# Optimization experiments

Hardware: AMD Instinct MI355X
Metric: run time of the kernel (lower is better)

Reference implementation:

```python
import jax, jax.numpy as jnp
import numpy as np

N_NODES = 100000
N_EDGES = 1600000
NODE_DIM = 64
HIDDEN = 256
OUT_DIM = 64
BN_EPS = 1e-5


def setup_inputs() -> dict:
    key = jax.random.key(0)
    ks = jax.random.split(key, 6)
    h = jax.random.normal(ks[0], (N_NODES, NODE_DIM), dtype=jnp.float32)
    W1 = jax.random.normal(ks[1], (NODE_DIM, HIDDEN), dtype=jnp.float32) * 0.1
    b1 = jnp.zeros((HIDDEN,), dtype=jnp.float32)
    W2 = jax.random.normal(ks[2], (HIDDEN, OUT_DIM), dtype=jnp.float32) * 0.1
    b2 = jnp.zeros((OUT_DIM,), dtype=jnp.float32)
    gamma = jnp.ones((OUT_DIM,), dtype=jnp.float32)
    beta = jnp.zeros((OUT_DIM,), dtype=jnp.float32)
    src = jax.random.randint(ks[3], (N_EDGES,), 0, N_NODES, dtype=jnp.int32)
    dst = jax.random.randint(ks[4], (N_EDGES,), 0, N_NODES, dtype=jnp.int32)
    return {"h": h, "W1": W1, "b1": b1, "W2": W2, "b2": b2,
            "gamma": gamma, "beta": beta, "src": src, "dst": dst}


def reference(h, W1, b1, W2, b2, gamma, beta, src, dst):
    # --- mean aggregation over incoming neighbors (DGL update_all) ---
    # mailbox mean == segment_sum(h[src]) / in_degree(dst), zero for isolated nodes
    agg_sum = jax.ops.segment_sum(h[src], dst, num_segments=N_NODES)  # [N, d]
    deg = jax.ops.segment_sum(jnp.ones((src.shape[0],), h.dtype), dst,
                              num_segments=N_NODES)
    agg = agg_sum / jnp.clip(deg, 1.0, None)[:, None]
    x = agg + h  # GIN combine: aggregated msg + self feature
    # --- 2-layer MLP with relu, then final relu (node_update_fn) ---
    x = jax.nn.relu(x @ W1 + b1)
    x = x @ W2 + b2
    x = jax.nn.relu(x)
    # --- BatchNorm1d over node (batch) dimension, training-mode stats ---
    mean = jnp.mean(x, axis=0)
    var = jnp.var(x, axis=0)  # biased variance, as torch BN training
    x = (x - mean) * jax.lax.rsqrt(var + BN_EPS) * gamma + beta
    return x
```

## Files before the change

kernel.cpp:

```cpp
#include <hip/hip_runtime.h>

#define N_NODES 100000
#define N_EDGES 1600000
#define DIM     64
#define HID     256
#define BN_EPS  1e-5f

#define NBUCK   391
#define RSTRIDE 392
#define SCHUNK  3125
#define SBLK    512
#define MAXB    6144

#define XBROWS  100032
#define NGP     782
#define MLPGRID 256
#define MAXIT   4

typedef short bf16x8 __attribute__((ext_vector_type(8)));
typedef float f32x4  __attribute__((ext_vector_type(4)));


__device__ __forceinline__ unsigned short f2bf(float x) {
    unsigned int u = __float_as_uint(x);
    unsigned int r = (u + 0x7FFFu + ((u >> 16) & 1u)) >> 16;
    return (unsigned short)r;
}

#define WAITV(N) asm volatile("s_waitcnt vmcnt(" #N ")" ::: "memory")

__device__ __forceinline__ void stage_issue(const unsigned short* gsrc,
                                            unsigned short* ldst) {
    __builtin_amdgcn_global_load_lds(
        (const __attribute__((address_space(1))) void*)gsrc,
        (__attribute__((address_space(3))) void*)ldst, 16, 0, 0);
    __builtin_amdgcn_global_load_lds(
        (const __attribute__((address_space(1))) void*)(gsrc + 512),
        (__attribute__((address_space(3))) void*)(ldst + 512), 16, 0, 0);
}

__global__ __launch_bounds__(1024) void kA_scatter(const int* __restrict__ src,
                                                   const int* __restrict__ dst,
                                                   unsigned int* __restrict__ ebuf,
                                                   int* __restrict__ runoff) {
    __shared__ int hist[NBUCK];
    __shared__ int ebase[NBUCK];
    __shared__ int sc[512];
    __shared__ unsigned int stage[SCHUNK];
    const int t = threadIdx.x;
    const int e0 = blockIdx.x * SCHUNK;
    const int n = SCHUNK;

    for (int i = t; i < NBUCK; i += 1024) hist[i] = 0;
    __syncthreads();
    for (int i = t; i < n; i += 1024)
        atomicAdd(&hist[dst[e0 + i] >> 8], 1);
    __syncthreads();

    if (t < 512) sc[t] = (t < NBUCK) ? hist[t] : 0;
    __syncthreads();
    for (int off = 1; off < 512; off <<= 1) {
        int add = (t < 512 && t >= off) ? sc[t - off] : 0;
        __syncthreads();
        if (t < 512) sc[t] += add;
        __syncthreads();
    }
    if (t < NBUCK) {
        int ex = sc[t] - hist[t];
        ebase[t] = ex;
        runoff[blockIdx.x * RSTRIDE + t] = ex;
    }
    if (t == 0) runoff[blockIdx.x * RSTRIDE + NBUCK] = n;
    if (t < NBUCK) hist[t] = 0;
    __syncthreads();

    for (int i = t; i < n; i += 1024) {
        int d = dst[e0 + i];
        int s = src[e0 + i];
        int b = d >> 8;
        int r = atomicAdd(&hist[b], 1);
        stage[ebase[b] + r] = ((unsigned int)s << 8) | (unsigned int)(d & 255);
    }
    __syncthreads();
    for (int i = t; i < n; i += 1024)
        ebuf[e0 + i] = stage[i];
}

__global__ __launch_bounds__(1024) void kB_fused(const unsigned int* __restrict__ ebuf,
                                                 const int* __restrict__ runoff,
                                                 const unsigned short* __restrict__ hb,
                                                 unsigned short* __restrict__ xb) {
    __shared__ int runbase[SBLK + 1];
    __shared__ int runstart[SBLK];
    __shared__ int sc[SBLK];
    __shared__ int cnt[256];
    __shared__ int off[256];
    __shared__ unsigned int stage2[MAXB];
    __shared__ unsigned int sout[MAXB];
    const int t = threadIdx.x;
    const int b = blockIdx.x;

    int rl = 0;
    if (t < SBLK) {
        int s = runoff[t * RSTRIDE + b];
        int e = runoff[t * RSTRIDE + b + 1];
        runstart[t] = t * SCHUNK + s;
        rl = e - s;
        sc[t] = rl;
    }
    if (t < 256) cnt[t] = 0;
    __syncthreads();
    for (int o = 1; o < SBLK; o <<= 1) {
        int add = (t < SBLK && t >= o) ? sc[t - o] : 0;
        __syncthreads();
        if (t < SBLK) sc[t] += add;
        __syncthreads();
    }
    if (t < SBLK) runbase[t] = sc[t] - rl;
    if (t == 0) runbase[SBLK] = sc[SBLK - 1];
    __syncthreads();
    const int total = min(runbase[SBLK], MAXB);

    for (int idx = t; idx < total; idx += 1024) {
        int lo = 0, hi = SBLK - 1;
        while (lo < hi) {
            int mid = (lo + hi + 1) >> 1;
            if (runbase[mid] <= idx) lo = mid; else hi = mid - 1;
        }
        unsigned int v = ebuf[runstart[lo] + (idx - runbase[lo])];
        stage2[idx] = v;
        atomicAdd(&cnt[v & 255u], 1);
    }
    __syncthreads();

    int c0 = (t < 256) ? cnt[t] : 0;
    if (t < 256) sc[t] = c0;
    __syncthreads();
    for (int o = 1; o < 256; o <<= 1) {
        int add = (t < 256 && t >= o) ? sc[t - o] : 0;
        __syncthreads();
        if (t < 256) sc[t] += add;
        __syncthreads();
    }
    if (t < 256) { off[t] = sc[t] - c0; cnt[t] = 0; }
    __syncthreads();

    for (int idx = t; idx < total; idx += 1024) {
        unsigned int v = stage2[idx];
        int node = (int)(v & 255u);
        int r = atomicAdd(&cnt[node], 1);
        sout[off[node] + r] = v >> 8;
    }
    __syncthreads();

    const int g = t >> 3, c = t & 7;
    const unsigned short* hc = hb + c * 8;
    const int gn0 = b * 256;
#pragma unroll
    for (int pass = 0; pass < 2; ++pass) {
        int nloc = pass * 128 + g;
        int gnode = gn0 + nloc;
        if (gnode >= N_NODES) continue;
        const int o0 = off[nloc];
        const int dg = cnt[nloc];
        float a0 = 0.f, a1 = 0.f, a2 = 0.f, a3 = 0.f;
        float a4 = 0.f, a5 = 0.f, a6 = 0.f, a7 = 0.f;
        int j = 0;
        for (; j + 1 < dg; j += 2) {
            int i0 = (int)sout[o0 + j];
            int i1 = (int)sout[o0 + j + 1];
            uint4 v0 = *(const uint4*)&hc[(size_t)i0 * 64];
            uint4 v1 = *(const uint4*)&hc[(size_t)i1 * 64];
            a0 += __uint_as_float(v0.x << 16); a1 += __uint_as_float(v0.x & 0xffff0000u);
            a2 += __uint_as_float(v0.y << 16); a3 += __uint_as_float(v0.y & 0xffff0000u);
            a4 += __uint_as_float(v0.z << 16); a5 += __uint_as_float(v0.z & 0xffff0000u);
            a6 += __uint_as_float(v0.w << 16); a7 += __uint_as_float(v0.w & 0xffff0000u);
            a0 += __uint_as_float(v1.x << 16); a1 += __uint_as_float(v1.x & 0xffff0000u);
            a2 += __uint_as_float(v1.y << 16); a3 += __uint_as_float(v1.y & 0xffff0000u);
            a4 += __uint_as_float(v1.z << 16); a5 += __uint_as_float(v1.z & 0xffff0000u);
            a6 += __uint_as_float(v1.w << 16); a7 += __uint_as_float(v1.w & 0xffff0000u);
        }
        if (j < dg) {
            int i0 = (int)sout[o0 + j];
            uint4 v0 = *(const uint4*)&hc[(size_t)i0 * 64];
            a0 += __uint_as_float(v0.x << 16); a1 += __uint_as_float(v0.x & 0xffff0000u);
            a2 += __uint_as_float(v0.y << 16); a3 += __uint_as_float(v0.y & 0xffff0000u);
            a4 += __uint_as_float(v0.z << 16); a5 += __uint_as_float(v0.z & 0xffff0000u);
            a6 += __uint_as_float(v0.w << 16); a7 += __uint_as_float(v0.w & 0xffff0000u);
        }
        const float inv = 1.0f / (float)max(dg, 1);
        uint4 ov = *(const uint4*)&hc[(size_t)gnode * 64];
        float x0 = fmaf(a0, inv, __uint_as_float(ov.x << 16));
        float x1 = fmaf(a1, inv, __uint_as_float(ov.x & 0xffff0000u));
        float x2 = fmaf(a2, inv, __uint_as_float(ov.y << 16));
        float x3 = fmaf(a3, inv, __uint_as_float(ov.y & 0xffff0000u));
        float x4 = fmaf(a4, inv, __uint_as_float(ov.z << 16));
        float x5 = fmaf(a5, inv, __uint_as_float(ov.z & 0xffff0000u));
        float x6 = fmaf(a6, inv, __uint_as_float(ov.w << 16));
        float x7 = fmaf(a7, inv, __uint_as_float(ov.w & 0xffff0000u));
        uint4 o;
        o.x = (unsigned)f2bf(x0) | ((unsigned)f2bf(x1) << 16);
        o.y = (unsigned)f2bf(x2) | ((unsigned)f2bf(x3) << 16);
        o.z = (unsigned)f2bf(x4) | ((unsigned)f2bf(x5) << 16);
        o.w = (unsigned)f2bf(x6) | ((unsigned)f2bf(x7) << 16);
        *(uint4*)&xb[(size_t)gnode * 64 + ((c ^ (gnode & 7)) << 3)] = o;
    }
}

__global__ __launch_bounds__(256) void k_wprep(const float* __restrict__ W1,
                                               const float* __restrict__ W2,
                                               const float* __restrict__ h,
                                               unsigned short* __restrict__ w1t,
                                               unsigned short* __restrict__ w2t,
                                               unsigned short* __restrict__ xb,
                                               unsigned short* __restrict__ hb) {
    int id = blockIdx.x * 256 + threadIdx.x;
    if (id < 16384) {
        int n = id >> 6, k = id & 63;
        int dstp = (n << 6) + ((((k >> 3) ^ (n & 7))) << 3) + (k & 7);
        w1t[dstp] = f2bf(W1[k * 256 + n]);
    } else if (id < 32768) {
        int i2 = id - 16384;
        int d = i2 >> 8, k2 = i2 & 255;
        int dstp = (d << 8) + ((((k2 >> 3) ^ (d & 7))) << 3) + (k2 & 7);
        w2t[dstp] = f2bf(W2[k2 * 64 + d]);
    } else if (id < 34816) {
        xb[100000 * 64 + (id - 32768)] = 0;
    } else {
        int i = id - 34816;
        int e = i * 8;
        float4 f0 = *(const float4*)&h[e];
        float4 f1 = *(const float4*)&h[e + 4];
        uint4 o;
        o.x = (unsigned)f2bf(f0.x) | ((unsigned)f2bf(f0.y) << 16);
        o.y = (unsigned)f2bf(f0.z) | ((unsigned)f2bf(f0.w) << 16);
        o.z = (unsigned)f2bf(f1.x) | ((unsigned)f2bf(f1.y) << 16);
        o.w = (unsigned)f2bf(f1.z) | ((unsigned)f2bf(f1.w) << 16);
        *(uint4*)&hb[e] = o;
    }
}

__device__ __forceinline__ void mlp_tile(const unsigned short* sXw,
                                         const unsigned short* sW1,
                                         const unsigned short* sW2,
                                         unsigned short* sHw,
                                         const float* sB1,
                                         int l15, int g4, int s7,
                                         f32x4 oacc[4]) {
    bf16x8 xf0 = *(const bf16x8*)&sXw[l15 * 64 + ((g4 ^ s7) << 3)];
    bf16x8 xf1 = *(const bf16x8*)&sXw[l15 * 64 + (((g4 + 4) ^ s7) << 3)];
#pragma unroll
    for (int dt = 0; dt < 4; ++dt) oacc[dt] = (f32x4){0.f, 0.f, 0.f, 0.f};

#pragma unroll
    for (int p = 0; p < 4; ++p) {
#pragma unroll
        for (int nt2 = 0; nt2 < 4; ++nt2) {
            const int n0 = p * 64 + nt2 * 16;
            f32x4 hacc = (f32x4){0.f, 0.f, 0.f, 0.f};
            bf16x8 wf0 = *(const bf16x8*)&sW1[(n0 + l15) * 64 + ((g4 ^ s7) << 3)];
            bf16x8 wf1 = *(const bf16x8*)&sW1[(n0 + l15) * 64 + (((g4 + 4) ^ s7) << 3)];
            hacc = __builtin_amdgcn_mfma_f32_16x16x32_bf16(wf0, xf0, hacc, 0, 0, 0);
            hacc = __builtin_amdgcn_mfma_f32_16x16x32_bf16(wf1, xf1, hacc, 0, 0, 0);
            float4 bq = *(const float4*)&sB1[n0 + g4 * 4];
            ushort4 pk;
            pk.x = f2bf(fmaxf(hacc[0] + bq.x, 0.f));
            pk.y = f2bf(fmaxf(hacc[1] + bq.y, 0.f));
            pk.z = f2bf(fmaxf(hacc[2] + bq.z, 0.f));
            pk.w = f2bf(fmaxf(hacc[3] + bq.w, 0.f));
            int qh = nt2 * 2 + (g4 >> 1);
            *(ushort4*)&sHw[l15 * 64 + ((qh ^ s7) << 3) + ((g4 & 1) << 2)] = pk;
        }
#pragma unroll
        for (int s2 = 0; s2 < 2; ++s2) {
            bf16x8 a2 = *(const bf16x8*)&sHw[l15 * 64 + (((s2 * 4 + g4) ^ s7) << 3)];
#pragma unroll
            for (int dt = 0; dt < 4; ++dt) {
                int q = p * 8 + s2 * 4 + g4;
                bf16x8 w2f = *(const bf16x8*)&sW2[(dt * 16 + l15) * 256 + ((q ^ s7) << 3)];
                oacc[dt] = __builtin_amdgcn_mfma_f32_16x16x32_bf16(a2, w2f, oacc[dt], 0, 0, 0);
            }
        }
    }
}

__global__ __launch_bounds__(512, 2) void k_mlpf(const unsigned short* __restrict__ xb,
                                                 const unsigned short* __restrict__ w1t,
                                                 const unsigned short* __restrict__ w2t,
                                                 const float* __restrict__ b1,
                                                 const float* __restrict__ b2,
                                                 const float* __restrict__ gamma,
                                                 const float* __restrict__ beta,
                                                 float* __restrict__ stats,
                                                 int* __restrict__ bar,
                                                 float* __restrict__ out,
                                                 float* __restrict__ dump) {
    __shared__ unsigned short sW1[256 * 64];
    __shared__ unsigned short sW2[64 * 256];
    __shared__ unsigned short sH[8][16 * 64];
    __shared__ unsigned short sX[8][2][16 * 64];
    __shared__ float sB1[256];
    const int t = threadIdx.x;
    const int lane = t & 63;
    const int w = t >> 6;
    const int l15 = lane & 15;
    const int g4 = lane >> 4;
    const int s7 = l15 & 7;
    const int bid = blockIdx.x;

    for (int i = t; i < 2048; i += 512)
        *(uint4*)&sW1[i * 8] = *(const uint4*)&w1t[i * 8];
    for (int i = t; i < 2048; i += 512)
        *(uint4*)&sW2[i * 8] = *(const uint4*)&w2t[i * 8];
    if (t < 256) sB1[t] = b1[t];
    __syncthreads();

    float b2v[4];
#pragma unroll
    for (int dt = 0; dt < 4; ++dt) b2v[dt] = b2[dt * 16 + l15];

    float lsum[4] = {0.f, 0.f, 0.f, 0.f};
    float lsq[4]  = {0.f, 0.f, 0.f, 0.f};
    f32x4 osave[MAXIT][4];

    int cur = 0;
    {
        int r0 = min(bid * 128 + w * 16, XBROWS - 16);
        stage_issue(xb + (size_t)r0 * 64 + lane * 8, &sX[w][0][0]);
    }
#pragma unroll
    for (int it = 0; it < MAXIT; ++it) {
        int gp = bid + it * MLPGRID;
        int gpn = gp + MLPGRID; if (gpn >= NGP) gpn = gp;
        int r0n = min(gpn * 128 + w * 16, XBROWS - 16);
        stage_issue(xb + (size_t)r0n * 64 + lane * 8, &sX[w][cur ^ 1][0]);
        WAITV(2);
        __builtin_amdgcn_sched_barrier(0);
        const int row0 = gp * 128 + w * 16;
        if (gp < NGP && row0 < XBROWS) {
            f32x4 oacc[4];
            mlp_tile(&sX[w][cur][0], sW1, sW2, &sH[w][0], sB1, l15, g4, s7, oacc);
#pragma unroll
            for (int dt = 0; dt < 4; ++dt) {
#pragma unroll
                for (int r = 0; r < 4; ++r) {
                    float val = fmaxf(oacc[dt][r] + b2v[dt], 0.f);
                    osave[it][dt][r] = val;
                    int mabs = row0 + g4 * 4 + r;
                    if (mabs < N_NODES) {
                        lsum[dt] += val;
                        lsq[dt] += val * val;
                    }
                }
            }
        }
        cur ^= 1;
    }

    __syncthreads();
    float* sred = (float*)&sW1[0];
#pragma unroll
    for (int dt = 0; dt < 4; ++dt) {
        sred[t * 8 + dt] = lsum[dt];
        sred[t * 8 + 4 + dt] = lsq[dt];
    }
    __syncthreads();
    if (t < 128) {
        int issq = (t >= 64) ? 4 : 0;
        int d = t & 63;
        int dt = d >> 4, dl = d & 15;
        float acc = 0.f;
        for (int i = 0; i < 32; ++i) acc += sred[(dl + 16 * i) * 8 + issq + dt];
        atomicAdd(&stats[(issq ? 64 : 0) + d], acc);
    }

    __syncthreads();
    if (t == 0) {
        __hip_atomic_fetch_add(bar, 1, __ATOMIC_ACQ_REL, __HIP_MEMORY_SCOPE_AGENT);
        while (__hip_atomic_load(bar, __ATOMIC_ACQUIRE, __HIP_MEMORY_SCOPE_AGENT)
               < MLPGRID)
            __builtin_amdgcn_s_sleep(4);
    }
    __syncthreads();

    float scv[4], shv[4];
    const float inv_n = 1.0f / (float)N_NODES;
#pragma unroll
    for (int dt = 0; dt < 4; ++dt) {
        int d = dt * 16 + l15;
        float sm = __hip_atomic_load(&stats[d], __ATOMIC_RELAXED,
                                     __HIP_MEMORY_SCOPE_AGENT);
        float sq = __hip_atomic_load(&stats[64 + d], __ATOMIC_RELAXED,
                                     __HIP_MEMORY_SCOPE_AGENT);
        float m = sm * inv_n;
        float v = sq * inv_n - m * m;
        float sc = gamma[d] * rsqrtf(v + BN_EPS);
        scv[dt] = sc;
        shv[dt] = beta[d] - m * sc;
    }

#pragma unroll
    for (int it = 0; it < MAXIT; ++it) {
        int gp = bid + it * MLPGRID;
        const int row0 = gp * 128 + w * 16;
        if (gp >= NGP || row0 >= XBROWS) continue;
        float* sHf = (float*)&sH[w][0];
#pragma unroll
        for (int hh = 0; hh < 2; ++hh) {
            asm volatile("" ::: "memory");
            if ((g4 >> 1) == hh) {
#pragma unroll
                for (int dt = 0; dt < 4; ++dt) {
#pragma unroll
                    for (int r = 0; r < 4; ++r) {
                        float val = fmaf(osave[it][dt][r], scv[dt], shv[dt]);
                        sHf[((g4 & 1) * 4 + r) * 64 + dt * 16 + l15] = val;
                    }
                }
            }
            asm volatile("" ::: "memory");
#pragma unroll
            for (int j = 0; j < 2; ++j) {
                int rl = j * 4 + (lane >> 4);
                int rg = row0 + hh * 8 + rl;
                float4 v = *(const float4*)&sHf[rl * 64 + (lane & 15) * 4];
                float* dstp = (rg < N_NODES)
                    ? &out[(size_t)rg * 64 + (lane & 15) * 4]
                    : &dump[lane * 4];
                *(float4*)dstp = v;
            }
        }
    }
}

extern "C" void kernel_launch(void* const* d_in, const int* in_sizes, int n_in,
                              void* d_out, int out_size, void* d_ws, size_t ws_size,
                              hipStream_t stream) {
    const float* h     = (const float*)d_in[0];
    const float* W1    = (const float*)d_in[1];
    const float* b1    = (const float*)d_in[2];
    const float* W2    = (const float*)d_in[3];
    const float* b2    = (const float*)d_in[4];
    const float* gamma = (const float*)d_in[5];
    const float* beta  = (const float*)d_in[6];
    const int*   src   = (const int*)d_in[7];
    const int*   dst   = (const int*)d_in[8];

    int* wsi = (int*)d_ws;
    float*          stats  = (float*)wsi;
    int*            bar    = wsi + 128;
    int*            runoff = wsi + 256;
    float*          dump   = (float*)(wsi + 256);
    unsigned short* w1t    = (unsigned short*)(wsi + 200960);
    unsigned short* w2t    = (unsigned short*)(wsi + 209152);
    unsigned short* xb     = (unsigned short*)(wsi + 217344);
    unsigned int*   ebuf   = (unsigned int*)(wsi + 3418368);
    unsigned short* hb     = (unsigned short*)(wsi + 5018368);
    float*          out    = (float*)d_out;

    hipMemsetAsync(wsi, 0, 1024, stream);

    kA_scatter<<<SBLK, 1024, 0, stream>>>(src, dst, ebuf, runoff);
    k_wprep<<<3261, 256, 0, stream>>>(W1, W2, h, w1t, w2t, xb, hb);
    kB_fused<<<NBUCK, 1024, 0, stream>>>(ebuf, runoff, hb, xb);
    k_mlpf<<<MLPGRID, 512, 0, stream>>>(xb, w1t, w2t, b1, b2, gamma, beta,
                                        stats, bar, out, dump);
}
```

Measured before the change: 176.1 us.

## Fuse weight/feature prep and memset into scatter kernel; per-run copy in kB

Folds the bf16 conversion of h, the weight transposes, the xb padding zeroing and the stats/barrier memset into the edge-scatter kernel, removing one kernel launch and one memset. In kB_fused, each thread now copies its whole contiguous run instead of binary-searching the run for every element. f2bf switches to the compiler's native bf16 conversion with packed pairs. Per-run copying is serial per thread and may be unbalanced, and the extra work lengthens the scatter kernel's tail.

```diff
diff --git a/kernel.cpp b/kernel.cpp
--- a/kernel.cpp
+++ b/kernel.cpp
@@ -22,9 +22,12 @@
 
 
 __device__ __forceinline__ unsigned short f2bf(float x) {
-    unsigned int u = __float_as_uint(x);
-    unsigned int r = (u + 0x7FFFu + ((u >> 16) & 1u)) >> 16;
-    return (unsigned short)r;
+    union { __bf16 b; unsigned short u; } cv;
+    cv.b = (__bf16)x;
+    return cv.u;
+}
+__device__ __forceinline__ unsigned pk2(float a, float b) {
+    return (unsigned)f2bf(a) | ((unsigned)f2bf(b) << 16);
 }
 
 #define WAITV(N) asm volatile("s_waitcnt vmcnt(" #N ")" ::: "memory")
@@ -41,8 +44,16 @@
 
 __global__ __launch_bounds__(1024) void kA_scatter(const int* __restrict__ src,
                                                    const int* __restrict__ dst,
+                                                   const float* __restrict__ h,
+                                                   const float* __restrict__ W1,
+                                                   const float* __restrict__ W2,
                                                    unsigned int* __restrict__ ebuf,
-                                                   int* __restrict__ runoff) {
+                                                   int* __restrict__ runoff,
+                                                   unsigned short* __restrict__ w1t,
+                                                   unsigned short* __restrict__ w2t,
+                                                   unsigned short* __restrict__ xb,
+                                                   unsigned short* __restrict__ hb,
+                                                   int* __restrict__ statsbar) {
     __shared__ int hist[NBUCK];
     __shared__ int ebase[NBUCK];
     __shared__ int sc[512];
@@ -84,6 +95,32 @@
     __syncthreads();
     for (int i = t; i < n; i += 1024)
         ebuf[e0 + i] = stage[i];
+
+    for (int i = blockIdx.x * 1024 + t; i < 800000; i += SBLK * 1024) {
+        int e = i * 8;
+        float4 f0 = *(const float4*)&h[e];
+        float4 f1 = *(const float4*)&h[e + 4];
+        uint4 o;
+        o.x = pk2(f0.x, f0.y);
+        o.y = pk2(f0.z, f0.w);
+        o.z = pk2(f1.x, f1.y);
+        o.w = pk2(f1.z, f1.w);
+        *(uint4*)&hb[e] = o;
+    }
+    int id = blockIdx.x * 1024 + t;
+    if (id < 16384) {
+        int nn = id >> 6, k = id & 63;
+        int dstp = (nn << 6) + ((((k >> 3) ^ (nn & 7))) << 3) + (k & 7);
+        w1t[dstp] = f2bf(W1[k * 256 + nn]);
+    } else if (id < 32768) {
+        int i2 = id - 16384;
+        int d = i2 >> 8, k2 = i2 & 255;
+        int dstp = (d << 8) + ((((k2 >> 3) ^ (d & 7))) << 3) + (k2 & 7);
+        w2t[dstp] = f2bf(W2[k2 * 64 + d]);
+    } else if (id < 34816) {
+        xb[100000 * 64 + (id - 32768)] = 0;
+    }
+    if (blockIdx.x == 34 && t < 256) statsbar[t] = 0;
 }
 
 __global__ __launch_bounds__(1024) void kB_fused(const unsigned int* __restrict__ ebuf,
@@ -91,7 +128,6 @@
                                                  const unsigned short* __restrict__ hb,
                                                  unsigned short* __restrict__ xb) {
     __shared__ int runbase[SBLK + 1];
-    __shared__ int runstart[SBLK];
     __shared__ int sc[SBLK];
     __shared__ int cnt[256];
     __shared__ int off[256];
@@ -100,11 +136,11 @@
     const int t = threadIdx.x;
     const int b = blockIdx.x;
 
-    int rl = 0;
+    int rl = 0, rs = 0;
     if (t < SBLK) {
         int s = runoff[t * RSTRIDE + b];
         int e = runoff[t * RSTRIDE + b + 1];
-        runstart[t] = t * SCHUNK + s;
+        rs = t * SCHUNK + s;
         rl = e - s;
         sc[t] = rl;
     }
@@ -116,20 +152,18 @@
         if (t < SBLK) sc[t] += add;
         __syncthreads();
     }
-    if (t < SBLK) runbase[t] = sc[t] - rl;
     if (t == 0) runbase[SBLK] = sc[SBLK - 1];
     __syncthreads();
     const int total = min(runbase[SBLK], MAXB);
 
-    for (int idx = t; idx < total; idx += 1024) {
-        int lo = 0, hi = SBLK - 1;
-        while (lo < hi) {
-            int mid = (lo + hi + 1) >> 1;
-            if (runbase[mid] <= idx) lo = mid; else hi = mid - 1;
-        }
-        unsigned int v = ebuf[runstart[lo] + (idx - runbase[lo])];
-        stage2[idx] = v;
-        atomicAdd(&cnt[v & 255u], 1);
+    if (t < SBLK && rl > 0) {
+        int base = sc[t] - rl;
+        int lim = min(rl, MAXB - base);
+        for (int k = 0; k < lim; ++k) {
+            unsigned int v = ebuf[rs + k];
+            stage2[base + k] = v;
+            atomicAdd(&cnt[v & 255u], 1);
+        }
     }
     __syncthreads();
 
@@ -199,44 +233,11 @@
         float x6 = fmaf(a6, inv, __uint_as_float(ov.w << 16));
         float x7 = fmaf(a7, inv, __uint_as_float(ov.w & 0xffff0000u));
         uint4 o;
-        o.x = (unsigned)f2bf(x0) | ((unsigned)f2bf(x1) << 16);
-        o.y = (unsigned)f2bf(x2) | ((unsigned)f2bf(x3) << 16);
-        o.z = (unsigned)f2bf(x4) | ((unsigned)f2bf(x5) << 16);
-        o.w = (unsigned)f2bf(x6) | ((unsigned)f2bf(x7) << 16);
+        o.x = pk2(x0, x1);
+        o.y = pk2(x2, x3);
+        o.z = pk2(x4, x5);
+        o.w = pk2(x6, x7);
         *(uint4*)&xb[(size_t)gnode * 64 + ((c ^ (gnode & 7)) << 3)] = o;
-    }
-}
-
-__global__ __launch_bounds__(256) void k_wprep(const float* __restrict__ W1,
-                                               const float* __restrict__ W2,
-                                               const float* __restrict__ h,
-                                               unsigned short* __restrict__ w1t,
-                                               unsigned short* __restrict__ w2t,
-                                               unsigned short* __restrict__ xb,
-                                               unsigned short* __restrict__ hb) {
-    int id = blockIdx.x * 256 + threadIdx.x;
-    if (id < 16384) {
-        int n = id >> 6, k = id & 63;
-        int dstp = (n << 6) + ((((k >> 3) ^ (n & 7))) << 3) + (k & 7);
-        w1t[dstp] = f2bf(W1[k * 256 + n]);
-    } else if (id < 32768) {
-        int i2 = id - 16384;
-        int d = i2 >> 8, k2 = i2 & 255;
-        int dstp = (d << 8) + ((((k2 >> 3) ^ (d & 7))) << 3) + (k2 & 7);
-        w2t[dstp] = f2bf(W2[k2 * 64 + d]);
-    } else if (id < 34816) {
-        xb[100000 * 64 + (id - 32768)] = 0;
-    } else {
-        int i = id - 34816;
-        int e = i * 8;
-        float4 f0 = *(const float4*)&h[e];
-        float4 f1 = *(const float4*)&h[e + 4];
-        uint4 o;
-        o.x = (unsigned)f2bf(f0.x) | ((unsigned)f2bf(f0.y) << 16);
-        o.y = (unsigned)f2bf(f0.z) | ((unsigned)f2bf(f0.w) << 16);
-        o.z = (unsigned)f2bf(f1.x) | ((unsigned)f2bf(f1.y) << 16);
-        o.w = (unsigned)f2bf(f1.z) | ((unsigned)f2bf(f1.w) << 16);
-        *(uint4*)&hb[e] = o;
     }
 }
 
@@ -263,13 +264,14 @@
             hacc = __builtin_amdgcn_mfma_f32_16x16x32_bf16(wf0, xf0, hacc, 0, 0, 0);
             hacc = __builtin_amdgcn_mfma_f32_16x16x32_bf16(wf1, xf1, hacc, 0, 0, 0);
             float4 bq = *(const float4*)&sB1[n0 + g4 * 4];
-            ushort4 pk;
-            pk.x = f2bf(fmaxf(hacc[0] + bq.x, 0.f));
-            pk.y = f2bf(fmaxf(hacc[1] + bq.y, 0.f));
-            pk.z = f2bf(fmaxf(hacc[2] + bq.z, 0.f));
-            pk.w = f2bf(fmaxf(hacc[3] + bq.w, 0.f));
+            ushort2 pkl, pkh;
+            unsigned plo = pk2(fmaxf(hacc[0] + bq.x, 0.f),
+                               fmaxf(hacc[1] + bq.y, 0.f));
+            unsigned phi = pk2(fmaxf(hacc[2] + bq.z, 0.f),
+                               fmaxf(hacc[3] + bq.w, 0.f));
             int qh = nt2 * 2 + (g4 >> 1);
-            *(ushort4*)&sHw[l15 * 64 + ((qh ^ s7) << 3) + ((g4 & 1) << 2)] = pk;
+            uint2 pk = {plo, phi};
+            *(uint2*)&sHw[l15 * 64 + ((qh ^ s7) << 3) + ((g4 & 1) << 2)] = pk;
         }
 #pragma unroll
         for (int s2 = 0; s2 < 2; ++s2) {
@@ -447,21 +449,20 @@
     const int*   dst   = (const int*)d_in[8];
 
     int* wsi = (int*)d_ws;
-    float*          stats  = (float*)wsi;
-    int*            bar    = wsi + 128;
-    int*            runoff = wsi + 256;
-    float*          dump   = (float*)(wsi + 256);
-    unsigned short* w1t    = (unsigned short*)(wsi + 200960);
-    unsigned short* w2t    = (unsigned short*)(wsi + 209152);
-    unsigned short* xb     = (unsigned short*)(wsi + 217344);
-    unsigned int*   ebuf   = (unsigned int*)(wsi + 3418368);
-    unsigned short* hb     = (unsigned short*)(wsi + 5018368);
-    float*          out    = (float*)d_out;
-
-    hipMemsetAsync(wsi, 0, 1024, stream);
-
-    kA_scatter<<<SBLK, 1024, 0, stream>>>(src, dst, ebuf, runoff);
-    k_wprep<<<3261, 256, 0, stream>>>(W1, W2, h, w1t, w2t, xb, hb);
+    float*          stats   = (float*)wsi;
+    int*            bar     = wsi + 128;
+    int*            statsbar = wsi;
+    int*            runoff  = wsi + 256;
+    float*          dump    = (float*)(wsi + 256);
+    unsigned short* w1t     = (unsigned short*)(wsi + 200960);
+    unsigned short* w2t     = (unsigned short*)(wsi + 209152);
+    unsigned short* xb      = (unsigned short*)(wsi + 217344);
+    unsigned int*   ebuf    = (unsigned int*)(wsi + 3418368);
+    unsigned short* hb      = (unsigned short*)(wsi + 5018368);
+    float*          out     = (float*)d_out;
+
+    kA_scatter<<<SBLK, 1024, 0, stream>>>(src, dst, h, W1, W2, ebuf, runoff,
+                                          w1t, w2t, xb, hb, statsbar);
     kB_fused<<<NBUCK, 1024, 0, stream>>>(ebuf, runoff, hb, xb);
     k_mlpf<<<MLPGRID, 512, 0, stream>>>(xb, w1t, w2t, b1, b2, gamma, beta,
                                         stats, bar, out, dump);
```

Measured after the change: 172.2 us. -2.2%, faster.
